# Kernel optimization log

Measured on AMD Instinct MI355X. Metric: run time of the kernel, lower is better.

Reference implementation:

```python
import jax, jax.numpy as jnp
import numpy as np

S = 512       # number of rnn_output rows (source positions)
T = 512       # number of target rows (queries)
DU = 512      # dim_u
DT = 512      # dim_target
D = DU + DT   # concat dim


def setup_inputs() -> dict:
    key = jax.random.key(0)
    k1, k2, k3, k4, k5, k6 = jax.random.split(key, 6)
    return {
        "rnn_outputs": jax.random.normal(k1, (S, DU), dtype=jnp.float32),
        "target": jax.random.normal(k2, (T, DT), dtype=jnp.float32),
        # nn.Linear(D, D): weight [D, D], bias [D]
        "W_lin": jax.random.normal(k3, (D, D), dtype=jnp.float32) * 0.02,
        "b_lin": jax.random.normal(k4, (D,), dtype=jnp.float32) * 0.02,
        # nn.Linear(D, 1): weight [1, D] stored flat, bias scalar
        "w_score": jax.random.normal(k5, (D,), dtype=jnp.float32) * 0.02,
        "b_score": jax.random.normal(k6, (), dtype=jnp.float32) * 0.02,
    }


def reference(rnn_outputs, target, W_lin, b_lin, w_score, b_score):
    du = rnn_outputs.shape[1]
    # linear(concat([rnn, tgt])) == rnn @ W[:, :du].T + tgt @ W[:, du:].T + b
    # (split the weight instead of materializing the [T, S, D] concat)
    A = rnn_outputs @ W_lin[:, :du].T            # [S, D]
    B = target @ W_lin[:, du:].T + b_lin         # [T, D]
    h = jnp.tanh(B[:, None, :] + A[None, :, :])  # [T, S, D]
    scores = h @ w_score + b_score               # [T, S]
    weights = jax.nn.softmax(scores, axis=1)     # softmax over source dim S
    # stack of per-row weighted sums == weights @ rnn_outputs
    return weights @ rnn_outputs                 # [T, dim_u]
```

## Files before the change

kernel.cpp:

```cpp
#include <hip/hip_runtime.h>


#define C2F 2.8853900817779268f

typedef __attribute__((ext_vector_type(8))) short short8;
typedef __attribute__((ext_vector_type(4))) float f32x4;
typedef __attribute__((ext_vector_type(2))) float f32x2;

__device__ __forceinline__ unsigned short bf16_rne(float f) {
    unsigned u = __builtin_bit_cast(unsigned, f);
    unsigned r = (u + 0x7FFFu + ((u >> 16) & 1u)) >> 16;
    return (unsigned short)r;
}
__device__ __forceinline__ float bf16_f(unsigned short h) {
    unsigned u = ((unsigned)h) << 16;
    return __builtin_bit_cast(float, u);
}
__device__ __forceinline__ f32x2 splat2(float s) {
    f32x2 r; r.x = s; r.y = s; return r;
}

__global__ __launch_bounds__(256, 4) void k1_mfma(
    const float* __restrict__ rnn, const float* __restrict__ tgt,
    const float* __restrict__ W, const float* __restrict__ bl,
    float* __restrict__ Abuf, float* __restrict__ Bbuf, int ksplit)
{
    __shared__ unsigned short Xh[64][40], Xl[64][40], Wh[64][40], Wl[64][40];
    const int j0 = blockIdx.x * 64;
    const int i0 = blockIdx.y * 64;
    const int kz = blockIdx.z;
    const int klen = 512 / ksplit;
    const int kbase = kz * klen;
    const bool isB = (i0 >= 512);
    const float* __restrict__ X = isB ? tgt : rnn;
    const int irow0 = isB ? (i0 - 512) : i0;
    const int koff = isB ? 512 : 0;
    const int tid = threadIdx.x;
    const int lane = tid & 63;
    const int wv = tid >> 6;
    const int isub = (wv & 1) * 32;
    const int jsub = (wv >> 1) * 32;
    const int srow = tid >> 2;
    const int skq  = tid & 3;
    const float* __restrict__ xp = X + (size_t)(irow0 + srow) * 512 + kbase + skq * 8;
    const float* __restrict__ wp = W + (size_t)(j0 + srow) * 1024 + koff + kbase + skq * 8;
    const int frow = lane & 15;
    const int fk   = (lane >> 4) * 8;
    f32x4 acc00 = {0.f,0.f,0.f,0.f}, acc01 = {0.f,0.f,0.f,0.f};
    f32x4 acc10 = {0.f,0.f,0.f,0.f}, acc11 = {0.f,0.f,0.f,0.f};
    float4 xv0 = *(const float4*)(xp);
    float4 xv1 = *(const float4*)(xp + 4);
    float4 wv0 = *(const float4*)(wp);
    float4 wv1 = *(const float4*)(wp + 4);
    for (int k0 = 0; k0 < klen; k0 += 32) {
        __syncthreads();
        {
            short8 xh8, xl8, wh8, wl8;
            const float xf[8] = {xv0.x, xv0.y, xv0.z, xv0.w, xv1.x, xv1.y, xv1.z, xv1.w};
            const float wf[8] = {wv0.x, wv0.y, wv0.z, wv0.w, wv1.x, wv1.y, wv1.z, wv1.w};
            #pragma unroll
            for (int e = 0; e < 8; ++e) {
                const unsigned short xh = bf16_rne(xf[e]);
                const unsigned short wh = bf16_rne(wf[e]);
                xh8[e] = (short)xh;
                wh8[e] = (short)wh;
                xl8[e] = (short)bf16_rne(xf[e] - bf16_f(xh));
                wl8[e] = (short)bf16_rne(wf[e] - bf16_f(wh));
            }
            *(short8*)&Xh[srow][skq * 8] = xh8;
            *(short8*)&Xl[srow][skq * 8] = xl8;
            *(short8*)&Wh[srow][skq * 8] = wh8;
            *(short8*)&Wl[srow][skq * 8] = wl8;
        }
        __syncthreads();
        if (k0 + 32 < klen) {
            xv0 = *(const float4*)(xp + k0 + 32);
            xv1 = *(const float4*)(xp + k0 + 36);
            wv0 = *(const float4*)(wp + k0 + 32);
            wv1 = *(const float4*)(wp + k0 + 36);
        }
        const short8 ah0 = *(const short8*)&Xh[isub + frow][fk];
        const short8 ah1 = *(const short8*)&Xh[isub + 16 + frow][fk];
        const short8 bh0 = *(const short8*)&Wh[jsub + frow][fk];
        const short8 bh1 = *(const short8*)&Wh[jsub + 16 + frow][fk];
        acc00 = __builtin_amdgcn_mfma_f32_16x16x32_bf16(ah0, bh0, acc00, 0, 0, 0);
        acc01 = __builtin_amdgcn_mfma_f32_16x16x32_bf16(ah0, bh1, acc01, 0, 0, 0);
        acc10 = __builtin_amdgcn_mfma_f32_16x16x32_bf16(ah1, bh0, acc10, 0, 0, 0);
        acc11 = __builtin_amdgcn_mfma_f32_16x16x32_bf16(ah1, bh1, acc11, 0, 0, 0);
        const short8 al0 = *(const short8*)&Xl[isub + frow][fk];
        const short8 al1 = *(const short8*)&Xl[isub + 16 + frow][fk];
        acc00 = __builtin_amdgcn_mfma_f32_16x16x32_bf16(al0, bh0, acc00, 0, 0, 0);
        acc01 = __builtin_amdgcn_mfma_f32_16x16x32_bf16(al0, bh1, acc01, 0, 0, 0);
        acc10 = __builtin_amdgcn_mfma_f32_16x16x32_bf16(al1, bh0, acc10, 0, 0, 0);
        acc11 = __builtin_amdgcn_mfma_f32_16x16x32_bf16(al1, bh1, acc11, 0, 0, 0);
        const short8 bl0 = *(const short8*)&Wl[jsub + frow][fk];
        const short8 bl1 = *(const short8*)&Wl[jsub + 16 + frow][fk];
        acc00 = __builtin_amdgcn_mfma_f32_16x16x32_bf16(ah0, bl0, acc00, 0, 0, 0);
        acc01 = __builtin_amdgcn_mfma_f32_16x16x32_bf16(ah0, bl1, acc01, 0, 0, 0);
        acc10 = __builtin_amdgcn_mfma_f32_16x16x32_bf16(ah1, bl0, acc10, 0, 0, 0);
        acc11 = __builtin_amdgcn_mfma_f32_16x16x32_bf16(ah1, bl1, acc11, 0, 0, 0);
    }
    const int orow = (lane >> 4) * 4;
    const int ocol = lane & 15;
    float* __restrict__ dst = (isB ? Bbuf : Abuf) + (size_t)kz * 524288;
    const bool addb = isB && (kz == ksplit - 1);
#define K1ST(ACC, MT, NT) do {                                            \
    const int jl = jsub + (NT)*16 + ocol;                                 \
    const float bb = addb ? bl[j0 + jl] : 0.f;                            \
    const int il = isub + (MT)*16 + orow;                                 \
    float* p = dst + (size_t)(irow0 + il) * 1024 + j0 + jl;               \
    p[0]    = (ACC[0] + bb) * C2F;                                        \
    p[1024] = (ACC[1] + bb) * C2F;                                        \
    p[2048] = (ACC[2] + bb) * C2F;                                        \
    p[3072] = (ACC[3] + bb) * C2F;                                        \
} while (0)
    K1ST(acc00, 0, 0); K1ST(acc01, 0, 1); K1ST(acc10, 1, 0); K1ST(acc11, 1, 1);
#undef K1ST
}

__global__ __launch_bounds__(256, 4) void k1_gemm_ab(
    const float* __restrict__ rnn, const float* __restrict__ tgt,
    const float* __restrict__ W, const float* __restrict__ bl,
    float* __restrict__ Abuf, float* __restrict__ Bbuf, int ksplit, int doexp)
{
    __shared__ float xt[32][68];
    __shared__ float wt[32][68];
    const int j0 = blockIdx.x * 64;
    const int i0 = blockIdx.y * 64;
    const int kz = blockIdx.z;
    const int klen = 512 / ksplit;
    const int kbase = kz * klen;
    const bool isB = (i0 >= 512);
    const float* __restrict__ in = isB ? tgt : rnn;
    const int irow0 = isB ? (i0 - 512) : i0;
    const int koff = isB ? 512 : 0;
    const int tid = threadIdx.x;
    const int lrow = tid >> 2;
    const int kq   = tid & 3;
    const int ti   = tid >> 4;
    const int tj   = tid & 15;
    const float* __restrict__ inp = in + (size_t)(irow0 + lrow) * 512 + kbase + kq * 8;
    const float* __restrict__ wp  = W  + (size_t)(j0 + lrow) * 1024 + koff + kbase + kq * 8;
    float acc[4][4] = {};
    float4 x0 = *(const float4*)(inp);
    float4 x1 = *(const float4*)(inp + 4);
    float4 w0 = *(const float4*)(wp);
    float4 w1 = *(const float4*)(wp + 4);
    for (int k0 = 0; k0 < klen; k0 += 32) {
        __syncthreads();
        xt[kq*8+0][lrow] = x0.x; xt[kq*8+1][lrow] = x0.y; xt[kq*8+2][lrow] = x0.z; xt[kq*8+3][lrow] = x0.w;
        xt[kq*8+4][lrow] = x1.x; xt[kq*8+5][lrow] = x1.y; xt[kq*8+6][lrow] = x1.z; xt[kq*8+7][lrow] = x1.w;
        wt[kq*8+0][lrow] = w0.x; wt[kq*8+1][lrow] = w0.y; wt[kq*8+2][lrow] = w0.z; wt[kq*8+3][lrow] = w0.w;
        wt[kq*8+4][lrow] = w1.x; wt[kq*8+5][lrow] = w1.y; wt[kq*8+6][lrow] = w1.z; wt[kq*8+7][lrow] = w1.w;
        __syncthreads();
        if (k0 + 32 < klen) {
            x0 = *(const float4*)(inp + k0 + 32);
            x1 = *(const float4*)(inp + k0 + 36);
            w0 = *(const float4*)(wp + k0 + 32);
            w1 = *(const float4*)(wp + k0 + 36);
        }
        #pragma unroll
        for (int k = 0; k < 32; ++k) {
            const float4 av = *(const float4*)&xt[k][ti * 4];
            const float4 bv = *(const float4*)&wt[k][tj * 4];
            const float ar[4] = {av.x, av.y, av.z, av.w};
            const float br[4] = {bv.x, bv.y, bv.z, bv.w};
            #pragma unroll
            for (int r = 0; r < 4; ++r)
                #pragma unroll
                for (int c = 0; c < 4; ++c)
                    acc[r][c] = __builtin_fmaf(ar[r], br[c], acc[r][c]);
        }
    }
    float4 bq = make_float4(0.f, 0.f, 0.f, 0.f);
    if (isB && kz == ksplit - 1) bq = *(const float4*)(bl + j0 + tj * 4);
    float* __restrict__ dst = (isB ? Bbuf : Abuf) + (size_t)kz * 524288;
    #pragma unroll
    for (int r = 0; r < 4; ++r) {
        float4 o;
        o.x = (acc[r][0] + bq.x) * C2F;
        o.y = (acc[r][1] + bq.y) * C2F;
        o.z = (acc[r][2] + bq.z) * C2F;
        o.w = (acc[r][3] + bq.w) * C2F;
        if (doexp) {
            o.x = __builtin_amdgcn_exp2f(o.x);
            o.y = __builtin_amdgcn_exp2f(o.y);
            o.z = __builtin_amdgcn_exp2f(o.z);
            o.w = __builtin_amdgcn_exp2f(o.w);
        }
        *(float4*)(dst + (size_t)(irow0 + ti * 4 + r) * 1024 + j0 + tj * 4) = o;
    }
}

#define K2P(ACC, PP, RR) do {                                                  \
    const f32x2 e0_ = __builtin_elementwise_fma(A0.PP, splat2(B0.RR), one2);   \
    const f32x2 e1_ = __builtin_elementwise_fma(A1.PP, splat2(B1.RR), one2);   \
    const f32x2 e2_ = __builtin_elementwise_fma(A2.PP, splat2(B2.RR), one2);   \
    const f32x2 e3_ = __builtin_elementwise_fma(A3.PP, splat2(B3.RR), one2);   \
    const f32x2 l01_ = e0_ * e1_;                                              \
    const f32x2 l23_ = e2_ * e3_;                                              \
    const f32x2 n01_ = __builtin_elementwise_fma(wx2, e1_, wy2 * e0_);         \
    const f32x2 n23_ = __builtin_elementwise_fma(wz2, e3_, ww2 * e2_);         \
    const f32x2 N_   = __builtin_elementwise_fma(n01_, l23_, n23_ * l01_);     \
    const f32x2 D_   = l01_ * l23_;                                            \
    f32x2 rd_;                                                                 \
    rd_.x = __builtin_amdgcn_rcpf(D_.x);                                       \
    rd_.y = __builtin_amdgcn_rcpf(D_.y);                                       \
    ACC = __builtin_elementwise_fma(N_, rd_, ACC);                             \
} while (0)

#define K2EXP(P0, P1) __builtin_amdgcn_exp2f(__builtin_fmaf(sumf, (P1), (P0)))

__global__ __launch_bounds__(256, 4) void k2_scores(
    const float* __restrict__ A0p, const float* __restrict__ A1p,
    const float* __restrict__ B0p, const float* __restrict__ B1p,
    const float* __restrict__ wsc, float* __restrict__ P, int dchunk, float sumf)
{
    __shared__ float at[32][68];
    __shared__ float bt[32][68];
    __shared__ float wl[128];
    const int s0 = blockIdx.x * 64;
    const int t0 = blockIdx.y * 64;
    const int dz = blockIdx.z * dchunk;
    const int tid = threadIdx.x;
    if (tid < dchunk) wl[tid] = wsc[dz + tid];
    const int srow = tid & 63;
    const int kq   = tid >> 6;
    const int ti   = tid >> 4;
    const int tj   = tid & 15;
    const float* __restrict__ Ar0 = A0p + (size_t)(s0 + srow) * 1024 + dz + kq * 8;
    const float* __restrict__ Ar1 = A1p + (size_t)(s0 + srow) * 1024 + dz + kq * 8;
    const float* __restrict__ Br0 = B0p + (size_t)(t0 + srow) * 1024 + dz + kq * 8;
    const float* __restrict__ Br1 = B1p + (size_t)(t0 + srow) * 1024 + dz + kq * 8;
    const f32x2 one2 = splat2(1.f);
    f32x2 ac0l = splat2(0.f), ac0h = splat2(0.f);
    f32x2 ac1l = splat2(0.f), ac1h = splat2(0.f);
    f32x2 ac2l = splat2(0.f), ac2h = splat2(0.f);
    f32x2 ac3l = splat2(0.f), ac3h = splat2(0.f);
    float4 pa0 = *(const float4*)(Ar0);
    float4 pa0b = *(const float4*)(Ar0 + 4);
    float4 pa1 = *(const float4*)(Ar1);
    float4 pa1b = *(const float4*)(Ar1 + 4);
    float4 pb0 = *(const float4*)(Br0);
    float4 pb0b = *(const float4*)(Br0 + 4);
    float4 pb1 = *(const float4*)(Br1);
    float4 pb1b = *(const float4*)(Br1 + 4);
    for (int d0 = 0; d0 < dchunk; d0 += 32) {
        __syncthreads();
        at[kq*8+0][srow] = K2EXP(pa0.x,  pa1.x);
        at[kq*8+1][srow] = K2EXP(pa0.y,  pa1.y);
        at[kq*8+2][srow] = K2EXP(pa0.z,  pa1.z);
        at[kq*8+3][srow] = K2EXP(pa0.w,  pa1.w);
        at[kq*8+4][srow] = K2EXP(pa0b.x, pa1b.x);
        at[kq*8+5][srow] = K2EXP(pa0b.y, pa1b.y);
        at[kq*8+6][srow] = K2EXP(pa0b.z, pa1b.z);
        at[kq*8+7][srow] = K2EXP(pa0b.w, pa1b.w);
        bt[kq*8+0][srow] = K2EXP(pb0.x,  pb1.x);
        bt[kq*8+1][srow] = K2EXP(pb0.y,  pb1.y);
        bt[kq*8+2][srow] = K2EXP(pb0.z,  pb1.z);
        bt[kq*8+3][srow] = K2EXP(pb0.w,  pb1.w);
        bt[kq*8+4][srow] = K2EXP(pb0b.x, pb1b.x);
        bt[kq*8+5][srow] = K2EXP(pb0b.y, pb1b.y);
        bt[kq*8+6][srow] = K2EXP(pb0b.z, pb1b.z);
        bt[kq*8+7][srow] = K2EXP(pb0b.w, pb1b.w);
        __syncthreads();
        if (d0 + 32 < dchunk) {
            pa0  = *(const float4*)(Ar0 + d0 + 32);
            pa0b = *(const float4*)(Ar0 + d0 + 36);
            pa1  = *(const float4*)(Ar1 + d0 + 32);
            pa1b = *(const float4*)(Ar1 + d0 + 36);
            pb0  = *(const float4*)(Br0 + d0 + 32);
            pb0b = *(const float4*)(Br0 + d0 + 36);
            pb1  = *(const float4*)(Br1 + d0 + 32);
            pb1b = *(const float4*)(Br1 + d0 + 36);
        }
        for (int dd = 0; dd < 32; dd += 4) {
            const float4 wa = *(const float4*)&wl[d0 + dd];
            const f32x2 wx2 = splat2(wa.x);
            const f32x2 wy2 = splat2(wa.y);
            const f32x2 wz2 = splat2(wa.z);
            const f32x2 ww2 = splat2(wa.w);
            const f32x4 A0 = *(const f32x4*)&at[dd + 0][tj * 4];
            const f32x4 A1 = *(const f32x4*)&at[dd + 1][tj * 4];
            const f32x4 A2 = *(const f32x4*)&at[dd + 2][tj * 4];
            const f32x4 A3 = *(const f32x4*)&at[dd + 3][tj * 4];
            const f32x4 B0 = *(const f32x4*)&bt[dd + 0][ti * 4];
            const f32x4 B1 = *(const f32x4*)&bt[dd + 1][ti * 4];
            const f32x4 B2 = *(const f32x4*)&bt[dd + 2][ti * 4];
            const f32x4 B3 = *(const f32x4*)&bt[dd + 3][ti * 4];
            K2P(ac0l, xy, x); K2P(ac0h, zw, x);
            K2P(ac1l, xy, y); K2P(ac1h, zw, y);
            K2P(ac2l, xy, z); K2P(ac2h, zw, z);
            K2P(ac3l, xy, w); K2P(ac3h, zw, w);
        }
    }
    float* __restrict__ Pz = P + (size_t)blockIdx.z * 512 * 512;
    float4 o0, o1, o2, o3;
    o0.x = ac0l.x; o0.y = ac0l.y; o0.z = ac0h.x; o0.w = ac0h.y;
    o1.x = ac1l.x; o1.y = ac1l.y; o1.z = ac1h.x; o1.w = ac1h.y;
    o2.x = ac2l.x; o2.y = ac2l.y; o2.z = ac2h.x; o2.w = ac2h.y;
    o3.x = ac3l.x; o3.y = ac3l.y; o3.z = ac3h.x; o3.w = ac3h.y;
    *(float4*)(Pz + (size_t)(t0 + ti * 4 + 0) * 512 + s0 + tj * 4) = o0;
    *(float4*)(Pz + (size_t)(t0 + ti * 4 + 1) * 512 + s0 + tj * 4) = o1;
    *(float4*)(Pz + (size_t)(t0 + ti * 4 + 2) * 512 + s0 + tj * 4) = o2;
    *(float4*)(Pz + (size_t)(t0 + ti * 4 + 3) * 512 + s0 + tj * 4) = o3;
}

__global__ __launch_bounds__(256, 4) void k3_softmax(
    const float* __restrict__ P, float* __restrict__ wgt, int nz)
{
    __shared__ float wm[4];
    __shared__ float wsum[4];
    const int t = blockIdx.x;
    const int tid = threadIdx.x;
    const size_t base = (size_t)t * 512 + tid * 2;
    float sx = 0.f, sy = 0.f;
    for (int z = 0; z < nz; ++z) {
        const float2 p = *(const float2*)(P + base + (size_t)z * 262144);
        sx += p.x; sy += p.y;
    }
    const float x0 = -2.f * sx;
    const float x1 = -2.f * sy;
    float m = fmaxf(x0, x1);
    #pragma unroll
    for (int off = 32; off; off >>= 1) m = fmaxf(m, __shfl_xor(m, off));
    if ((tid & 63) == 0) wm[tid >> 6] = m;
    __syncthreads();
    m = fmaxf(fmaxf(wm[0], wm[1]), fmaxf(wm[2], wm[3]));
    const float L2E = 1.4426950408889634f;
    const float e0 = __builtin_amdgcn_exp2f((x0 - m) * L2E);
    const float e1 = __builtin_amdgcn_exp2f((x1 - m) * L2E);
    float s = e0 + e1;
    #pragma unroll
    for (int off = 32; off; off >>= 1) s += __shfl_xor(s, off);
    if ((tid & 63) == 0) wsum[tid >> 6] = s;
    __syncthreads();
    s = wsum[0] + wsum[1] + wsum[2] + wsum[3];
    const float inv = 1.0f / s;
    float2 o; o.x = e0 * inv; o.y = e1 * inv;
    *(float2*)(wgt + (size_t)t * 512 + tid * 2) = o;
}

#define K4BFRAG(BH, BL, DCOL) do {                                      \
    _Pragma("unroll")                                                   \
    for (int e = 0; e < 8; ++e) {                                       \
        const float v_ = rs[fk + e][(DCOL)];                            \
        const unsigned short h_ = bf16_rne(v_);                         \
        (BH)[e] = (short)h_;                                            \
        (BL)[e] = (short)bf16_rne(v_ - bf16_f(h_));                     \
    }                                                                   \
} while (0)

__global__ __launch_bounds__(256, 4) void k4_mfma(
    const float* __restrict__ wgt, const float* __restrict__ rnn,
    float* __restrict__ P4)
{
    __shared__ unsigned short Gh[64][40], Gl[64][40];
    __shared__ float rs[32][69];
    const int d0g = blockIdx.x * 64;
    const int t0g = blockIdx.y * 64;
    const int z   = blockIdx.z;
    const int tid = threadIdx.x;
    const int lane = tid & 63;
    const int wv = tid >> 6;
    const int tsub = (wv & 1) * 32;
    const int dsub = (wv >> 1) * 32;
    const int trow = tid >> 2, skq = tid & 3;
    const int srw  = tid >> 3, cq  = tid & 7;
    const int frow = lane & 15;
    const int fk   = (lane >> 4) * 8;
    const int sbase = z * 64;
    f32x4 acc00 = {0.f,0.f,0.f,0.f}, acc01 = {0.f,0.f,0.f,0.f};
    f32x4 acc10 = {0.f,0.f,0.f,0.f}, acc11 = {0.f,0.f,0.f,0.f};
    const float* __restrict__ gp = wgt + (size_t)(t0g + trow) * 512 + sbase + skq * 8;
    const float* __restrict__ rp = rnn + (size_t)(sbase + srw) * 512 + d0g + cq * 8;
    float4 g0 = *(const float4*)(gp);
    float4 g1 = *(const float4*)(gp + 4);
    float4 r0 = *(const float4*)(rp);
    float4 r1 = *(const float4*)(rp + 4);
    #pragma unroll
    for (int c = 0; c < 2; ++c) {
        __syncthreads();
        {
            short8 gh8, gl8;
            const float gf[8] = {g0.x,g0.y,g0.z,g0.w,g1.x,g1.y,g1.z,g1.w};
            #pragma unroll
            for (int e = 0; e < 8; ++e) {
                const unsigned short h = bf16_rne(gf[e]);
                gh8[e] = (short)h;
                gl8[e] = (short)bf16_rne(gf[e] - bf16_f(h));
            }
            *(short8*)&Gh[trow][skq * 8] = gh8;
            *(short8*)&Gl[trow][skq * 8] = gl8;
            *(float4*)&rs[srw][cq * 8]     = r0;
            *(float4*)&rs[srw][cq * 8 + 4] = r1;
        }
        __syncthreads();
        if (c == 0) {
            g0 = *(const float4*)(gp + 32);
            g1 = *(const float4*)(gp + 36);
            r0 = *(const float4*)(rp + 32 * 512);
            r1 = *(const float4*)(rp + 32 * 512 + 4);
        }
        const short8 ah0 = *(const short8*)&Gh[tsub + frow][fk];
        const short8 ah1 = *(const short8*)&Gh[tsub + 16 + frow][fk];
        const short8 al0 = *(const short8*)&Gl[tsub + frow][fk];
        const short8 al1 = *(const short8*)&Gl[tsub + 16 + frow][fk];
        short8 bh0, bl0, bh1, bl1;
        K4BFRAG(bh0, bl0, dsub + frow);
        K4BFRAG(bh1, bl1, dsub + 16 + frow);
        acc00 = __builtin_amdgcn_mfma_f32_16x16x32_bf16(ah0, bh0, acc00, 0, 0, 0);
        acc01 = __builtin_amdgcn_mfma_f32_16x16x32_bf16(ah0, bh1, acc01, 0, 0, 0);
        acc10 = __builtin_amdgcn_mfma_f32_16x16x32_bf16(ah1, bh0, acc10, 0, 0, 0);
        acc11 = __builtin_amdgcn_mfma_f32_16x16x32_bf16(ah1, bh1, acc11, 0, 0, 0);
        acc00 = __builtin_amdgcn_mfma_f32_16x16x32_bf16(al0, bh0, acc00, 0, 0, 0);
        acc01 = __builtin_amdgcn_mfma_f32_16x16x32_bf16(al0, bh1, acc01, 0, 0, 0);
        acc10 = __builtin_amdgcn_mfma_f32_16x16x32_bf16(al1, bh0, acc10, 0, 0, 0);
        acc11 = __builtin_amdgcn_mfma_f32_16x16x32_bf16(al1, bh1, acc11, 0, 0, 0);
        acc00 = __builtin_amdgcn_mfma_f32_16x16x32_bf16(ah0, bl0, acc00, 0, 0, 0);
        acc01 = __builtin_amdgcn_mfma_f32_16x16x32_bf16(ah0, bl1, acc01, 0, 0, 0);
        acc10 = __builtin_amdgcn_mfma_f32_16x16x32_bf16(ah1, bl0, acc10, 0, 0, 0);
        acc11 = __builtin_amdgcn_mfma_f32_16x16x32_bf16(ah1, bl1, acc11, 0, 0, 0);
    }
    const int orow = (lane >> 4) * 4;
    const int ocol = lane & 15;
    float* __restrict__ Pz = P4 + (size_t)z * 262144;
#define K4ST(ACC, MT, NT) do {                                           \
    const int tl = tsub + (MT)*16 + orow;                                \
    const int dl = dsub + (NT)*16 + ocol;                                \
    float* p = Pz + (size_t)(t0g + tl) * 512 + d0g + dl;                 \
    p[0]    = ACC[0];                                                    \
    p[512]  = ACC[1];                                                    \
    p[1024] = ACC[2];                                                    \
    p[1536] = ACC[3];                                                    \
} while (0)
    K4ST(acc00, 0, 0); K4ST(acc01, 0, 1); K4ST(acc10, 1, 0); K4ST(acc11, 1, 1);
#undef K4ST
}

__global__ __launch_bounds__(256, 4) void k5_reduce(
    const float* __restrict__ P4, float* __restrict__ out)
{
    const int i = (blockIdx.x * 256 + threadIdx.x) * 4;
    float4 a = *(const float4*)(P4 + i);
    #pragma unroll
    for (int z = 1; z < 8; ++z) {
        const float4 b = *(const float4*)(P4 + (size_t)z * 262144 + i);
        a.x += b.x; a.y += b.y; a.z += b.z; a.w += b.w;
    }
    *(float4*)(out + i) = a;
}

extern "C" void kernel_launch(void* const* d_in, const int* in_sizes, int n_in,
                              void* d_out, int out_size, void* d_ws, size_t ws_size,
                              hipStream_t stream) {
    const float* rnn = (const float*)d_in[0];
    const float* tgt = (const float*)d_in[1];
    const float* W   = (const float*)d_in[2];
    const float* bl  = (const float*)d_in[3];
    const float* wsc = (const float*)d_in[4];
    float* out = (float*)d_out;

    const int nz = 8;
    const int dchunk = 1024 / nz;
    float* ws = (float*)d_ws;

    const bool split = (ws_size >= 17825792u);

    if (split) {
        float* A   = ws;
        float* B   = ws + 2 * 524288;
        float* P   = ws + 4 * 524288;
        float* wgt = P + (size_t)nz * 262144;
        float* P4  = P;
        k1_mfma   <<<dim3(16, 16, 2), 256, 0, stream>>>(rnn, tgt, W, bl, A, B, 2);
        k2_scores <<<dim3(8, 8, nz),  256, 0, stream>>>(A, A + 524288, B, B + 524288,
                                                        wsc, P, dchunk, 1.f);
        k3_softmax<<<512,             256, 0, stream>>>(P, wgt, nz);
        k4_mfma   <<<dim3(8, 8, 8),   256, 0, stream>>>(wgt, rnn, P4);
        k5_reduce <<<256,             256, 0, stream>>>(P4, out);
    } else {
        float* A   = ws;
        float* B   = ws + 524288;
        float* P   = ws + 2 * 524288;
        float* wgt = P + (size_t)nz * 262144;
        float* P4  = P;
        k1_gemm_ab<<<dim3(16, 16, 1), 256, 0, stream>>>(rnn, tgt, W, bl, A, B, 1, 0);
        k2_scores <<<dim3(8, 8, nz),  256, 0, stream>>>(A, A, B, B, wsc, P, dchunk, 0.f);
        k3_softmax<<<512,             256, 0, stream>>>(P, wgt, nz);
        k4_mfma   <<<dim3(8, 8, 8),   256, 0, stream>>>(wgt, rnn, P4);
        k5_reduce <<<256,             256, 0, stream>>>(P4, out);
    }
}
```

Baseline: 57.42 us.

## Double k2 staging chunk to 64 and drop register prefetch

The score kernel now stages 64 d-values per iteration instead of 32, so each thread loads 16 floats per operand and LDS tiles grow to 64x68. The software register prefetch of the next chunk is removed in favour of loading at the top of each iteration. This halves the number of barrier pairs per dchunk but exposes global load latency before the exp stage, and raises LDS use, which may cut occupancy.

```diff
diff --git a/kernel.cpp b/kernel.cpp
--- a/kernel.cpp
+++ b/kernel.cpp
@@ -216,8 +216,8 @@
     const float* __restrict__ B0p, const float* __restrict__ B1p,
     const float* __restrict__ wsc, float* __restrict__ P, int dchunk, float sumf)
 {
-    __shared__ float at[32][68];
-    __shared__ float bt[32][68];
+    __shared__ float at[64][68];
+    __shared__ float bt[64][68];
     __shared__ float wl[128];
     const int s0 = blockIdx.x * 64;
     const int t0 = blockIdx.y * 64;
@@ -228,54 +228,68 @@
     const int kq   = tid >> 6;
     const int ti   = tid >> 4;
     const int tj   = tid & 15;
-    const float* __restrict__ Ar0 = A0p + (size_t)(s0 + srow) * 1024 + dz + kq * 8;
-    const float* __restrict__ Ar1 = A1p + (size_t)(s0 + srow) * 1024 + dz + kq * 8;
-    const float* __restrict__ Br0 = B0p + (size_t)(t0 + srow) * 1024 + dz + kq * 8;
-    const float* __restrict__ Br1 = B1p + (size_t)(t0 + srow) * 1024 + dz + kq * 8;
+    const float* __restrict__ Ar0 = A0p + (size_t)(s0 + srow) * 1024 + dz + kq * 16;
+    const float* __restrict__ Ar1 = A1p + (size_t)(s0 + srow) * 1024 + dz + kq * 16;
+    const float* __restrict__ Br0 = B0p + (size_t)(t0 + srow) * 1024 + dz + kq * 16;
+    const float* __restrict__ Br1 = B1p + (size_t)(t0 + srow) * 1024 + dz + kq * 16;
     const f32x2 one2 = splat2(1.f);
     f32x2 ac0l = splat2(0.f), ac0h = splat2(0.f);
     f32x2 ac1l = splat2(0.f), ac1h = splat2(0.f);
     f32x2 ac2l = splat2(0.f), ac2h = splat2(0.f);
     f32x2 ac3l = splat2(0.f), ac3h = splat2(0.f);
-    float4 pa0 = *(const float4*)(Ar0);
-    float4 pa0b = *(const float4*)(Ar0 + 4);
-    float4 pa1 = *(const float4*)(Ar1);
-    float4 pa1b = *(const float4*)(Ar1 + 4);
-    float4 pb0 = *(const float4*)(Br0);
-    float4 pb0b = *(const float4*)(Br0 + 4);
-    float4 pb1 = *(const float4*)(Br1);
-    float4 pb1b = *(const float4*)(Br1 + 4);
-    for (int d0 = 0; d0 < dchunk; d0 += 32) {
-        __syncthreads();
-        at[kq*8+0][srow] = K2EXP(pa0.x,  pa1.x);
-        at[kq*8+1][srow] = K2EXP(pa0.y,  pa1.y);
-        at[kq*8+2][srow] = K2EXP(pa0.z,  pa1.z);
-        at[kq*8+3][srow] = K2EXP(pa0.w,  pa1.w);
-        at[kq*8+4][srow] = K2EXP(pa0b.x, pa1b.x);
-        at[kq*8+5][srow] = K2EXP(pa0b.y, pa1b.y);
-        at[kq*8+6][srow] = K2EXP(pa0b.z, pa1b.z);
-        at[kq*8+7][srow] = K2EXP(pa0b.w, pa1b.w);
-        bt[kq*8+0][srow] = K2EXP(pb0.x,  pb1.x);
-        bt[kq*8+1][srow] = K2EXP(pb0.y,  pb1.y);
-        bt[kq*8+2][srow] = K2EXP(pb0.z,  pb1.z);
-        bt[kq*8+3][srow] = K2EXP(pb0.w,  pb1.w);
-        bt[kq*8+4][srow] = K2EXP(pb0b.x, pb1b.x);
-        bt[kq*8+5][srow] = K2EXP(pb0b.y, pb1b.y);
-        bt[kq*8+6][srow] = K2EXP(pb0b.z, pb1b.z);
-        bt[kq*8+7][srow] = K2EXP(pb0b.w, pb1b.w);
-        __syncthreads();
-        if (d0 + 32 < dchunk) {
-            pa0  = *(const float4*)(Ar0 + d0 + 32);
-            pa0b = *(const float4*)(Ar0 + d0 + 36);
-            pa1  = *(const float4*)(Ar1 + d0 + 32);
-            pa1b = *(const float4*)(Ar1 + d0 + 36);
-            pb0  = *(const float4*)(Br0 + d0 + 32);
-            pb0b = *(const float4*)(Br0 + d0 + 36);
-            pb1  = *(const float4*)(Br1 + d0 + 32);
-            pb1b = *(const float4*)(Br1 + d0 + 36);
-        }
-        for (int dd = 0; dd < 32; dd += 4) {
-            const float4 wa = *(const float4*)&wl[d0 + dd];
+    for (int c0 = 0; c0 < dchunk; c0 += 64) {
+        const float4 a00 = *(const float4*)(Ar0 + c0);
+        const float4 a01 = *(const float4*)(Ar0 + c0 + 4);
+        const float4 a02 = *(const float4*)(Ar0 + c0 + 8);
+        const float4 a03 = *(const float4*)(Ar0 + c0 + 12);
+        const float4 a10 = *(const float4*)(Ar1 + c0);
+        const float4 a11 = *(const float4*)(Ar1 + c0 + 4);
+        const float4 a12 = *(const float4*)(Ar1 + c0 + 8);
+        const float4 a13 = *(const float4*)(Ar1 + c0 + 12);
+        const float4 b00 = *(const float4*)(Br0 + c0);
+        const float4 b01 = *(const float4*)(Br0 + c0 + 4);
+        const float4 b02 = *(const float4*)(Br0 + c0 + 8);
+        const float4 b03 = *(const float4*)(Br0 + c0 + 12);
+        const float4 b10 = *(const float4*)(Br1 + c0);
+        const float4 b11 = *(const float4*)(Br1 + c0 + 4);
+        const float4 b12 = *(const float4*)(Br1 + c0 + 8);
+        const float4 b13 = *(const float4*)(Br1 + c0 + 12);
+        __syncthreads();
+        at[kq*16+ 0][srow] = K2EXP(a00.x, a10.x);
+        at[kq*16+ 1][srow] = K2EXP(a00.y, a10.y);
+        at[kq*16+ 2][srow] = K2EXP(a00.z, a10.z);
+        at[kq*16+ 3][srow] = K2EXP(a00.w, a10.w);
+        at[kq*16+ 4][srow] = K2EXP(a01.x, a11.x);
+        at[kq*16+ 5][srow] = K2EXP(a01.y, a11.y);
+        at[kq*16+ 6][srow] = K2EXP(a01.z, a11.z);
+        at[kq*16+ 7][srow] = K2EXP(a01.w, a11.w);
+        at[kq*16+ 8][srow] = K2EXP(a02.x, a12.x);
+        at[kq*16+ 9][srow] = K2EXP(a02.y, a12.y);
+        at[kq*16+10][srow] = K2EXP(a02.z, a12.z);
+        at[kq*16+11][srow] = K2EXP(a02.w, a12.w);
+        at[kq*16+12][srow] = K2EXP(a03.x, a13.x);
+        at[kq*16+13][srow] = K2EXP(a03.y, a13.y);
+        at[kq*16+14][srow] = K2EXP(a03.z, a13.z);
+        at[kq*16+15][srow] = K2EXP(a03.w, a13.w);
+        bt[kq*16+ 0][srow] = K2EXP(b00.x, b10.x);
+        bt[kq*16+ 1][srow] = K2EXP(b00.y, b10.y);
+        bt[kq*16+ 2][srow] = K2EXP(b00.z, b10.z);
+        bt[kq*16+ 3][srow] = K2EXP(b00.w, b10.w);
+        bt[kq*16+ 4][srow] = K2EXP(b01.x, b11.x);
+        bt[kq*16+ 5][srow] = K2EXP(b01.y, b11.y);
+        bt[kq*16+ 6][srow] = K2EXP(b01.z, b11.z);
+        bt[kq*16+ 7][srow] = K2EXP(b01.w, b11.w);
+        bt[kq*16+ 8][srow] = K2EXP(b02.x, b12.x);
+        bt[kq*16+ 9][srow] = K2EXP(b02.y, b12.y);
+        bt[kq*16+10][srow] = K2EXP(b02.z, b12.z);
+        bt[kq*16+11][srow] = K2EXP(b02.w, b12.w);
+        bt[kq*16+12][srow] = K2EXP(b03.x, b13.x);
+        bt[kq*16+13][srow] = K2EXP(b03.y, b13.y);
+        bt[kq*16+14][srow] = K2EXP(b03.z, b13.z);
+        bt[kq*16+15][srow] = K2EXP(b03.w, b13.w);
+        __syncthreads();
+        for (int dd = 0; dd < 64; dd += 4) {
+            const float4 wa = *(const float4*)&wl[c0 + dd];
             const f32x2 wx2 = splat2(wa.x);
             const f32x2 wy2 = splat2(wa.y);
             const f32x2 wz2 = splat2(wa.z);
```

New measurement: 59.70 us. 4.0% more time.

## Store A/B transposed and precompute exp in a separate sum kernel

Applied to the files above, without the earlier changes.

The MFMA projection kernel now writes A and B transposed ([D][S] layout) with float4 stores, and a new elementwise kernel sums the split-K partials and applies exp2 once per element instead of inside every score tile. The score kernel then loads the pre-exponentiated transposed tiles directly into shared memory with vector stores, removing the transpose scatter and the repeated exp work. The cost is an extra kernel launch and an extra read/write pass over A and B. The fallback path now also uses the MFMA kernel, and the old FMA GEMM is removed.

```diff
diff --git a/kernel.cpp b/kernel.cpp
--- a/kernel.cpp
+++ b/kernel.cpp
@@ -108,88 +108,37 @@
     const int jl = jsub + (NT)*16 + ocol;                                 \
     const float bb = addb ? bl[j0 + jl] : 0.f;                            \
     const int il = isub + (MT)*16 + orow;                                 \
-    float* p = dst + (size_t)(irow0 + il) * 1024 + j0 + jl;               \
-    p[0]    = (ACC[0] + bb) * C2F;                                        \
-    p[1024] = (ACC[1] + bb) * C2F;                                        \
-    p[2048] = (ACC[2] + bb) * C2F;                                        \
-    p[3072] = (ACC[3] + bb) * C2F;                                        \
+    float4 o;                                                             \
+    o.x = (ACC[0] + bb) * C2F;                                            \
+    o.y = (ACC[1] + bb) * C2F;                                            \
+    o.z = (ACC[2] + bb) * C2F;                                            \
+    o.w = (ACC[3] + bb) * C2F;                                            \
+    *(float4*)(dst + (size_t)(j0 + jl) * 512 + irow0 + il) = o;           \
 } while (0)
     K1ST(acc00, 0, 0); K1ST(acc01, 0, 1); K1ST(acc10, 1, 0); K1ST(acc11, 1, 1);
 #undef K1ST
 }
 
-__global__ __launch_bounds__(256, 4) void k1_gemm_ab(
-    const float* __restrict__ rnn, const float* __restrict__ tgt,
-    const float* __restrict__ W, const float* __restrict__ bl,
-    float* __restrict__ Abuf, float* __restrict__ Bbuf, int ksplit, int doexp)
-{
-    __shared__ float xt[32][68];
-    __shared__ float wt[32][68];
-    const int j0 = blockIdx.x * 64;
-    const int i0 = blockIdx.y * 64;
-    const int kz = blockIdx.z;
-    const int klen = 512 / ksplit;
-    const int kbase = kz * klen;
-    const bool isB = (i0 >= 512);
-    const float* __restrict__ in = isB ? tgt : rnn;
-    const int irow0 = isB ? (i0 - 512) : i0;
-    const int koff = isB ? 512 : 0;
-    const int tid = threadIdx.x;
-    const int lrow = tid >> 2;
-    const int kq   = tid & 3;
-    const int ti   = tid >> 4;
-    const int tj   = tid & 15;
-    const float* __restrict__ inp = in + (size_t)(irow0 + lrow) * 512 + kbase + kq * 8;
-    const float* __restrict__ wp  = W  + (size_t)(j0 + lrow) * 1024 + koff + kbase + kq * 8;
-    float acc[4][4] = {};
-    float4 x0 = *(const float4*)(inp);
-    float4 x1 = *(const float4*)(inp + 4);
-    float4 w0 = *(const float4*)(wp);
-    float4 w1 = *(const float4*)(wp + 4);
-    for (int k0 = 0; k0 < klen; k0 += 32) {
-        __syncthreads();
-        xt[kq*8+0][lrow] = x0.x; xt[kq*8+1][lrow] = x0.y; xt[kq*8+2][lrow] = x0.z; xt[kq*8+3][lrow] = x0.w;
-        xt[kq*8+4][lrow] = x1.x; xt[kq*8+5][lrow] = x1.y; xt[kq*8+6][lrow] = x1.z; xt[kq*8+7][lrow] = x1.w;
-        wt[kq*8+0][lrow] = w0.x; wt[kq*8+1][lrow] = w0.y; wt[kq*8+2][lrow] = w0.z; wt[kq*8+3][lrow] = w0.w;
-        wt[kq*8+4][lrow] = w1.x; wt[kq*8+5][lrow] = w1.y; wt[kq*8+6][lrow] = w1.z; wt[kq*8+7][lrow] = w1.w;
-        __syncthreads();
-        if (k0 + 32 < klen) {
-            x0 = *(const float4*)(inp + k0 + 32);
-            x1 = *(const float4*)(inp + k0 + 36);
-            w0 = *(const float4*)(wp + k0 + 32);
-            w1 = *(const float4*)(wp + k0 + 36);
-        }
-        #pragma unroll
-        for (int k = 0; k < 32; ++k) {
-            const float4 av = *(const float4*)&xt[k][ti * 4];
-            const float4 bv = *(const float4*)&wt[k][tj * 4];
-            const float ar[4] = {av.x, av.y, av.z, av.w};
-            const float br[4] = {bv.x, bv.y, bv.z, bv.w};
-            #pragma unroll
-            for (int r = 0; r < 4; ++r)
-                #pragma unroll
-                for (int c = 0; c < 4; ++c)
-                    acc[r][c] = __builtin_fmaf(ar[r], br[c], acc[r][c]);
-        }
-    }
-    float4 bq = make_float4(0.f, 0.f, 0.f, 0.f);
-    if (isB && kz == ksplit - 1) bq = *(const float4*)(bl + j0 + tj * 4);
-    float* __restrict__ dst = (isB ? Bbuf : Abuf) + (size_t)kz * 524288;
-    #pragma unroll
-    for (int r = 0; r < 4; ++r) {
-        float4 o;
-        o.x = (acc[r][0] + bq.x) * C2F;
-        o.y = (acc[r][1] + bq.y) * C2F;
-        o.z = (acc[r][2] + bq.z) * C2F;
-        o.w = (acc[r][3] + bq.w) * C2F;
-        if (doexp) {
-            o.x = __builtin_amdgcn_exp2f(o.x);
-            o.y = __builtin_amdgcn_exp2f(o.y);
-            o.z = __builtin_amdgcn_exp2f(o.z);
-            o.w = __builtin_amdgcn_exp2f(o.w);
-        }
-        *(float4*)(dst + (size_t)(irow0 + ti * 4 + r) * 1024 + j0 + tj * 4) = o;
-    }
+__global__ __launch_bounds__(256, 4) void k1b_sum(
+    float* __restrict__ A0, const float* __restrict__ A1,
+    float* __restrict__ B0, const float* __restrict__ B1, float scale)
+{
+    const int i = (blockIdx.x * 256 + threadIdx.x) * 4;
+    const float4 a0 = *(const float4*)(A0 + i);
+    const float4 a1 = *(const float4*)(A1 + i);
+    const float4 b0 = *(const float4*)(B0 + i);
+    const float4 b1 = *(const float4*)(B1 + i);
+    float4 a, b;
+    a.x = __builtin_amdgcn_exp2f(__builtin_fmaf(scale, a1.x, a0.x));
+    a.y = __builtin_amdgcn_exp2f(__builtin_fmaf(scale, a1.y, a0.y));
+    a.z = __builtin_amdgcn_exp2f(__builtin_fmaf(scale, a1.z, a0.z));
+    a.w = __builtin_amdgcn_exp2f(__builtin_fmaf(scale, a1.w, a0.w));
+    b.x = __builtin_amdgcn_exp2f(__builtin_fmaf(scale, b1.x, b0.x));
+    b.y = __builtin_amdgcn_exp2f(__builtin_fmaf(scale, b1.y, b0.y));
+    b.z = __builtin_amdgcn_exp2f(__builtin_fmaf(scale, b1.z, b0.z));
+    b.w = __builtin_amdgcn_exp2f(__builtin_fmaf(scale, b1.w, b0.w));
+    *(float4*)(A0 + i) = a;
+    *(float4*)(B0 + i) = b;
 }
 
 #define K2P(ACC, PP, RR) do {                                                  \
@@ -209,12 +158,9 @@
     ACC = __builtin_elementwise_fma(N_, rd_, ACC);                             \
 } while (0)
 
-#define K2EXP(P0, P1) __builtin_amdgcn_exp2f(__builtin_fmaf(sumf, (P1), (P0)))
-
 __global__ __launch_bounds__(256, 4) void k2_scores(
-    const float* __restrict__ A0p, const float* __restrict__ A1p,
-    const float* __restrict__ B0p, const float* __restrict__ B1p,
-    const float* __restrict__ wsc, float* __restrict__ P, int dchunk, float sumf)
+    const float* __restrict__ EAT, const float* __restrict__ EBT,
+    const float* __restrict__ wsc, float* __restrict__ P, int dchunk)
 {
     __shared__ float at[32][68];
     __shared__ float bt[32][68];
@@ -224,58 +170,36 @@
     const int dz = blockIdx.z * dchunk;
     const int tid = threadIdx.x;
     if (tid < dchunk) wl[tid] = wsc[dz + tid];
-    const int srow = tid & 63;
-    const int kq   = tid >> 6;
+    const int drow = tid >> 3;
+    const int sc8  = (tid & 7) * 8;
     const int ti   = tid >> 4;
     const int tj   = tid & 15;
-    const float* __restrict__ Ar0 = A0p + (size_t)(s0 + srow) * 1024 + dz + kq * 8;
-    const float* __restrict__ Ar1 = A1p + (size_t)(s0 + srow) * 1024 + dz + kq * 8;
-    const float* __restrict__ Br0 = B0p + (size_t)(t0 + srow) * 1024 + dz + kq * 8;
-    const float* __restrict__ Br1 = B1p + (size_t)(t0 + srow) * 1024 + dz + kq * 8;
+    const float* __restrict__ Arow = EAT + (size_t)(dz + drow) * 512 + s0 + sc8;
+    const float* __restrict__ Brow = EBT + (size_t)(dz + drow) * 512 + t0 + sc8;
     const f32x2 one2 = splat2(1.f);
     f32x2 ac0l = splat2(0.f), ac0h = splat2(0.f);
     f32x2 ac1l = splat2(0.f), ac1h = splat2(0.f);
     f32x2 ac2l = splat2(0.f), ac2h = splat2(0.f);
     f32x2 ac3l = splat2(0.f), ac3h = splat2(0.f);
-    float4 pa0 = *(const float4*)(Ar0);
-    float4 pa0b = *(const float4*)(Ar0 + 4);
-    float4 pa1 = *(const float4*)(Ar1);
-    float4 pa1b = *(const float4*)(Ar1 + 4);
-    float4 pb0 = *(const float4*)(Br0);
-    float4 pb0b = *(const float4*)(Br0 + 4);
-    float4 pb1 = *(const float4*)(Br1);
-    float4 pb1b = *(const float4*)(Br1 + 4);
-    for (int d0 = 0; d0 < dchunk; d0 += 32) {
-        __syncthreads();
-        at[kq*8+0][srow] = K2EXP(pa0.x,  pa1.x);
-        at[kq*8+1][srow] = K2EXP(pa0.y,  pa1.y);
-        at[kq*8+2][srow] = K2EXP(pa0.z,  pa1.z);
-        at[kq*8+3][srow] = K2EXP(pa0.w,  pa1.w);
-        at[kq*8+4][srow] = K2EXP(pa0b.x, pa1b.x);
-        at[kq*8+5][srow] = K2EXP(pa0b.y, pa1b.y);
-        at[kq*8+6][srow] = K2EXP(pa0b.z, pa1b.z);
-        at[kq*8+7][srow] = K2EXP(pa0b.w, pa1b.w);
-        bt[kq*8+0][srow] = K2EXP(pb0.x,  pb1.x);
-        bt[kq*8+1][srow] = K2EXP(pb0.y,  pb1.y);
-        bt[kq*8+2][srow] = K2EXP(pb0.z,  pb1.z);
-        bt[kq*8+3][srow] = K2EXP(pb0.w,  pb1.w);
-        bt[kq*8+4][srow] = K2EXP(pb0b.x, pb1b.x);
-        bt[kq*8+5][srow] = K2EXP(pb0b.y, pb1b.y);
-        bt[kq*8+6][srow] = K2EXP(pb0b.z, pb1b.z);
-        bt[kq*8+7][srow] = K2EXP(pb0b.w, pb1b.w);
-        __syncthreads();
-        if (d0 + 32 < dchunk) {
-            pa0  = *(const float4*)(Ar0 + d0 + 32);
-            pa0b = *(const float4*)(Ar0 + d0 + 36);
-            pa1  = *(const float4*)(Ar1 + d0 + 32);
-            pa1b = *(const float4*)(Ar1 + d0 + 36);
-            pb0  = *(const float4*)(Br0 + d0 + 32);
-            pb0b = *(const float4*)(Br0 + d0 + 36);
-            pb1  = *(const float4*)(Br1 + d0 + 32);
-            pb1b = *(const float4*)(Br1 + d0 + 36);
+    float4 pa0 = *(const float4*)(Arow);
+    float4 pa1 = *(const float4*)(Arow + 4);
+    float4 pb0 = *(const float4*)(Brow);
+    float4 pb1 = *(const float4*)(Brow + 4);
+    for (int c0 = 0; c0 < dchunk; c0 += 32) {
+        __syncthreads();
+        *(float4*)&at[drow][sc8]     = pa0;
+        *(float4*)&at[drow][sc8 + 4] = pa1;
+        *(float4*)&bt[drow][sc8]     = pb0;
+        *(float4*)&bt[drow][sc8 + 4] = pb1;
+        __syncthreads();
+        if (c0 + 32 < dchunk) {
+            pa0 = *(const float4*)(Arow + (size_t)(c0 + 32) * 512);
+            pa1 = *(const float4*)(Arow + (size_t)(c0 + 32) * 512 + 4);
+            pb0 = *(const float4*)(Brow + (size_t)(c0 + 32) * 512);
+            pb1 = *(const float4*)(Brow + (size_t)(c0 + 32) * 512 + 4);
         }
         for (int dd = 0; dd < 32; dd += 4) {
-            const float4 wa = *(const float4*)&wl[d0 + dd];
+            const float4 wa = *(const float4*)&wl[c0 + dd];
             const f32x2 wx2 = splat2(wa.x);
             const f32x2 wy2 = splat2(wa.y);
             const f32x2 wz2 = splat2(wa.z);
@@ -474,8 +398,8 @@
         float* wgt = P + (size_t)nz * 262144;
         float* P4  = P;
         k1_mfma   <<<dim3(16, 16, 2), 256, 0, stream>>>(rnn, tgt, W, bl, A, B, 2);
-        k2_scores <<<dim3(8, 8, nz),  256, 0, stream>>>(A, A + 524288, B, B + 524288,
-                                                        wsc, P, dchunk, 1.f);
+        k1b_sum   <<<512,             256, 0, stream>>>(A, A + 524288, B, B + 524288, 1.f);
+        k2_scores <<<dim3(8, 8, nz),  256, 0, stream>>>(A, B, wsc, P, dchunk);
         k3_softmax<<<512,             256, 0, stream>>>(P, wgt, nz);
         k4_mfma   <<<dim3(8, 8, 8),   256, 0, stream>>>(wgt, rnn, P4);
         k5_reduce <<<256,             256, 0, stream>>>(P4, out);
@@ -485,8 +409,9 @@
         float* P   = ws + 2 * 524288;
         float* wgt = P + (size_t)nz * 262144;
         float* P4  = P;
-        k1_gemm_ab<<<dim3(16, 16, 1), 256, 0, stream>>>(rnn, tgt, W, bl, A, B, 1, 0);
-        k2_scores <<<dim3(8, 8, nz),  256, 0, stream>>>(A, A, B, B, wsc, P, dchunk, 0.f);
+        k1_mfma   <<<dim3(16, 16, 1), 256, 0, stream>>>(rnn, tgt, W, bl, A, B, 1);
+        k1b_sum   <<<512,             256, 0, stream>>>(A, A, B, B, 0.f);
+        k2_scores <<<dim3(8, 8, nz),  256, 0, stream>>>(A, B, wsc, P, dchunk);
         k3_softmax<<<512,             256, 0, stream>>>(P, wgt, nz);
         k4_mfma   <<<dim3(8, 8, 8),   256, 0, stream>>>(wgt, rnn, P4);
         k5_reduce <<<256,             256, 0, stream>>>(P4, out);
```

Result: no change. 58.01 us (+1.0%).
